# Performance work log

Measured on AMD Instinct MI355X. Metric: run time of the kernel, lower is better.

## Reference

```python
import jax, jax.numpy as jnp
import numpy as np

N_ATOMS = 50000
N_EDGES = 640000
RBF_DIM = 64
HIDDEN = 128


def setup_inputs() -> dict:
    key = jax.random.key(0)
    ks = jax.random.split(key, 12)
    s = 0.05
    return {
        "atom_feat": jax.random.normal(ks[0], (N_ATOMS, HIDDEN), jnp.float32),
        "pair_feat": jax.random.normal(ks[1], (N_EDGES, RBF_DIM), jnp.float32),
        "recv_idx": jax.random.randint(ks[2], (N_EDGES,), 0, N_ATOMS, jnp.int32),
        # dense_rbf: rbf_dim -> hidden
        "w_rbf": jax.random.normal(ks[3], (RBF_DIM, HIDDEN), jnp.float32) * s,
        "b_rbf": jnp.zeros((HIDDEN,), jnp.float32),
        # dense_pair: hidden -> hidden
        "w_pair": jax.random.normal(ks[4], (HIDDEN, HIDDEN), jnp.float32) * s,
        "b_pair": jnp.zeros((HIDDEN,), jnp.float32),
        # atom MLP: hidden -> hidden (swish) -> hidden
        "w1": jax.random.normal(ks[5], (HIDDEN, HIDDEN), jnp.float32) * s,
        "b1": jnp.zeros((HIDDEN,), jnp.float32),
        "w2": jax.random.normal(ks[6], (HIDDEN, HIDDEN), jnp.float32) * s,
        "b2": jnp.zeros((HIDDEN,), jnp.float32),
    }


def reference(atom_feat, pair_feat, recv_idx, w_rbf, b_rbf, w_pair, b_pair, w1, b1, w2, b2):
    # edge MLP: two linear layers (no activation, matching keras Dense defaults)
    edge_messages = pair_feat @ w_rbf + b_rbf            # [E, H]
    edge_messages = edge_messages @ w_pair + b_pair      # [E, H]
    # scatter-add edge messages onto receiving atoms
    aggregated = jax.ops.segment_sum(edge_messages, recv_idx, num_segments=atom_feat.shape[0])  # [N, H]
    # atom MLP with swish hidden activation + residual
    h = jax.nn.silu(aggregated @ w1 + b1)
    return atom_feat + (h @ w2 + b2)
```

## Files before the change

kernel.cpp:

```cpp
#include <hip/hip_runtime.h>
#include <hip/hip_bf16.h>

#define HID 128
#define RBF 64
#define CAP 40
#define APB 16

typedef __attribute__((ext_vector_type(8))) __bf16 bf16x8;
typedef __attribute__((ext_vector_type(4))) float  f32x4;

__device__ __forceinline__ int pack_off(int k, int j) {
    return (((k >> 5) * HID + j) * 4 + ((k >> 3) & 3)) * 8 + (k & 7);
}

__global__ __launch_bounds__(256) void k_prep(
    const float* __restrict__ w_rbf, const float* __restrict__ b_rbf,
    const float* __restrict__ w_pair, const float* __restrict__ b_pair,
    const float* __restrict__ w1, const float* __restrict__ w2,
    __bf16* __restrict__ wcp, float* __restrict__ b_comb,
    __bf16* __restrict__ w1p, __bf16* __restrict__ w2p,
    int* __restrict__ counts, int N)
{
    const int n4 = (N + 3) >> 2;
    const int e_zero = n4;
    const int e_wc   = e_zero + RBF * HID;
    const int e_bc   = e_wc + HID;
    const int e_w1   = e_bc + HID * HID;
    const int e_w2   = e_w1 + HID * HID;

    for (int i = blockIdx.x * 256 + threadIdx.x; i < e_w2; i += gridDim.x * 256) {
        if (i < e_zero) {
            int base = i * 4;
            if (base + 3 < N) reinterpret_cast<int4*>(counts)[i] = make_int4(0, 0, 0, 0);
            else for (int t = base; t < N; ++t) counts[t] = 0;
        } else if (i < e_wc) {
            int tid = i - e_zero;
            int k = tid >> 7, j = tid & (HID - 1);
            float acc = 0.f;
            #pragma unroll 8
            for (int l = 0; l < HID; ++l) acc += w_rbf[k * HID + l] * w_pair[l * HID + j];
            wcp[pack_off(k, j)] = (__bf16)acc;
        } else if (i < e_bc) {
            int j = i - e_wc;
            float acc = b_pair[j];
            #pragma unroll 8
            for (int l = 0; l < HID; ++l) acc += b_rbf[l] * w_pair[l * HID + j];
            b_comb[j] = acc;
        } else if (i < e_w1) {
            int tid = i - e_bc;
            int k = tid >> 7, j = tid & (HID - 1);
            w1p[pack_off(k, j)] = (__bf16)w1[tid];
        } else {
            int tid = i - e_w1;
            int k = tid >> 7, j = tid & (HID - 1);
            w2p[pack_off(k, j)] = (__bf16)w2[tid];
        }
    }
}

__global__ __launch_bounds__(256) void k_fill(
    const int* __restrict__ recv, int* counts, int* __restrict__ edge_list, int E)
{
    int e = blockIdx.x * 256 + threadIdx.x;
    if (e < E) {
        int r = recv[e];
        int slot = atomicAdd(&counts[r], 1);
        if (slot < CAP) edge_list[(size_t)r * CAP + slot] = e;
    }
}

__global__ __launch_bounds__(256) void k_fused(
    const float* __restrict__ pair_feat, const float* __restrict__ atom_feat,
    const int* __restrict__ counts, const int* __restrict__ edge_list,
    const __bf16* __restrict__ wcp, const float* __restrict__ bc,
    const __bf16* __restrict__ w1p, const float* __restrict__ b1,
    const __bf16* __restrict__ w2p, const float* __restrict__ b2,
    float* __restrict__ out, int n_atoms)
{
    __shared__ __bf16 s_lds[APB][RBF + 8];
    __shared__ __bf16 x_lds[APB][HID + 8];

    const int tid  = threadIdx.x;
    const int lane = tid & 63;
    const int wv   = tid >> 6;
    const int lo   = lane & 15;
    const int hi   = lane >> 4;
    const int a0   = blockIdx.x * APB;

    const int ab = a0 + wv * 4;
    int dq[4], eidq[4];
    #pragma unroll
    for (int q = 0; q < 4; ++q) {
        int a = ab + q;
        dq[q]   = (a < n_atoms) ? counts[a] : 0;
        eidq[q] = (lane < CAP && a < n_atoms) ? edge_list[(size_t)a * CAP + lane] : 0;
    }

    #pragma unroll
    for (int q = 0; q < 4; ++q) {
        int d = dq[q]; if (d > CAP) d = CAP;
        int eid = eidq[q];

        float acc0 = 0.f, acc1 = 0.f, acc2 = 0.f, acc3 = 0.f;
        float acc4 = 0.f, acc5 = 0.f, acc6 = 0.f, acc7 = 0.f;
        int p = 0;
        for (; p + 8 <= d; p += 8) {
            int e0 = __shfl(eid, p),     e1 = __shfl(eid, p + 1);
            int e2 = __shfl(eid, p + 2), e3 = __shfl(eid, p + 3);
            int e4 = __shfl(eid, p + 4), e5 = __shfl(eid, p + 5);
            int e6 = __shfl(eid, p + 6), e7 = __shfl(eid, p + 7);
            acc0 += pair_feat[(size_t)e0 * RBF + lane];
            acc1 += pair_feat[(size_t)e1 * RBF + lane];
            acc2 += pair_feat[(size_t)e2 * RBF + lane];
            acc3 += pair_feat[(size_t)e3 * RBF + lane];
            acc4 += pair_feat[(size_t)e4 * RBF + lane];
            acc5 += pair_feat[(size_t)e5 * RBF + lane];
            acc6 += pair_feat[(size_t)e6 * RBF + lane];
            acc7 += pair_feat[(size_t)e7 * RBF + lane];
        }
        if (p + 4 <= d) {
            int e0 = __shfl(eid, p),     e1 = __shfl(eid, p + 1);
            int e2 = __shfl(eid, p + 2), e3 = __shfl(eid, p + 3);
            acc0 += pair_feat[(size_t)e0 * RBF + lane];
            acc1 += pair_feat[(size_t)e1 * RBF + lane];
            acc2 += pair_feat[(size_t)e2 * RBF + lane];
            acc3 += pair_feat[(size_t)e3 * RBF + lane];
            p += 4;
        }
        if (p + 2 <= d) {
            int e0 = __shfl(eid, p), e1 = __shfl(eid, p + 1);
            acc4 += pair_feat[(size_t)e0 * RBF + lane];
            acc5 += pair_feat[(size_t)e1 * RBF + lane];
            p += 2;
        }
        if (p < d) {
            int e0 = __shfl(eid, p);
            acc6 += pair_feat[(size_t)e0 * RBF + lane];
        }
        s_lds[wv * 4 + q][lane] =
            (__bf16)(((acc0 + acc1) + (acc2 + acc3)) + ((acc4 + acc5) + (acc6 + acc7)));
    }
    __syncthreads();

    float dg[4];
    #pragma unroll
    for (int j = 0; j < 4; ++j) {
        int a = a0 + hi * 4 + j;
        dg[j] = (a < n_atoms) ? (float)counts[a] : 0.f;
    }

    bf16x8 sa0 = *reinterpret_cast<const bf16x8*>(&s_lds[lo][hi * 8]);
    bf16x8 sa1 = *reinterpret_cast<const bf16x8*>(&s_lds[lo][32 + hi * 8]);

    f32x4 acc[2];

    #pragma unroll
    for (int c = 0; c < 2; ++c) {
        int col = (wv * 2 + c) * 16 + lo;
        float bcv = bc[col];
        acc[c] = (f32x4){dg[0] * bcv, dg[1] * bcv, dg[2] * bcv, dg[3] * bcv};
        bf16x8 wb0 = *reinterpret_cast<const bf16x8*>(wcp + ((size_t)(0 * HID + col) * 4 + hi) * 8);
        bf16x8 wb1 = *reinterpret_cast<const bf16x8*>(wcp + ((size_t)(1 * HID + col) * 4 + hi) * 8);
        acc[c] = __builtin_amdgcn_mfma_f32_16x16x32_bf16(sa0, wb0, acc[c], 0, 0, 0);
        acc[c] = __builtin_amdgcn_mfma_f32_16x16x32_bf16(sa1, wb1, acc[c], 0, 0, 0);
    }
    #pragma unroll
    for (int c = 0; c < 2; ++c)
        #pragma unroll
        for (int j = 0; j < 4; ++j)
            x_lds[hi * 4 + j][(wv * 2 + c) * 16 + lo] = (__bf16)acc[c][j];
    __syncthreads();

    #pragma unroll
    for (int c = 0; c < 2; ++c) {
        float bv = b1[(wv * 2 + c) * 16 + lo];
        acc[c] = (f32x4){bv, bv, bv, bv};
    }
    #pragma unroll
    for (int t = 0; t < 4; ++t) {
        bf16x8 af = *reinterpret_cast<const bf16x8*>(&x_lds[lo][t * 32 + hi * 8]);
        #pragma unroll
        for (int c = 0; c < 2; ++c) {
            int col = (wv * 2 + c) * 16 + lo;
            bf16x8 bf = *reinterpret_cast<const bf16x8*>(
                w1p + ((size_t)(t * HID + col) * 4 + hi) * 8);
            acc[c] = __builtin_amdgcn_mfma_f32_16x16x32_bf16(af, bf, acc[c], 0, 0, 0);
        }
    }
    __syncthreads();

    #pragma unroll
    for (int c = 0; c < 2; ++c)
        #pragma unroll
        for (int j = 0; j < 4; ++j) {
            float z = acc[c][j];
            float h = z * (1.f / (1.f + __expf(-z)));
            x_lds[hi * 4 + j][(wv * 2 + c) * 16 + lo] = (__bf16)h;
        }
    __syncthreads();

    #pragma unroll
    for (int c = 0; c < 2; ++c) {
        float bv = b2[(wv * 2 + c) * 16 + lo];
        acc[c] = (f32x4){bv, bv, bv, bv};
    }
    #pragma unroll
    for (int t = 0; t < 4; ++t) {
        bf16x8 af = *reinterpret_cast<const bf16x8*>(&x_lds[lo][t * 32 + hi * 8]);
        #pragma unroll
        for (int c = 0; c < 2; ++c) {
            int col = (wv * 2 + c) * 16 + lo;
            bf16x8 bf = *reinterpret_cast<const bf16x8*>(
                w2p + ((size_t)(t * HID + col) * 4 + hi) * 8);
            acc[c] = __builtin_amdgcn_mfma_f32_16x16x32_bf16(af, bf, acc[c], 0, 0, 0);
        }
    }

    #pragma unroll
    for (int c = 0; c < 2; ++c)
        #pragma unroll
        for (int j = 0; j < 4; ++j) {
            int a = a0 + hi * 4 + j;
            if (a < n_atoms) {
                size_t idx = (size_t)a * HID + (wv * 2 + c) * 16 + lo;
                out[idx] = atom_feat[idx] + acc[c][j];
            }
        }
}

extern "C" void kernel_launch(void* const* d_in, const int* in_sizes, int n_in,
                              void* d_out, int out_size, void* d_ws, size_t ws_size,
                              hipStream_t stream)
{
    const float* atom_feat = (const float*)d_in[0];
    const float* pair_feat = (const float*)d_in[1];
    const int*   recv_idx  = (const int*)d_in[2];
    const float* w_rbf  = (const float*)d_in[3];
    const float* b_rbf  = (const float*)d_in[4];
    const float* w_pair = (const float*)d_in[5];
    const float* b_pair = (const float*)d_in[6];
    const float* w1     = (const float*)d_in[7];
    const float* b1     = (const float*)d_in[8];
    const float* w2     = (const float*)d_in[9];
    const float* b2     = (const float*)d_in[10];
    float* out = (float*)d_out;

    const int N = in_sizes[0] / HID;
    const int E = in_sizes[2];

    __bf16* wcp    = (__bf16*)d_ws;
    float*  b_comb = (float*)(wcp + RBF * HID);
    __bf16* w1p    = (__bf16*)(b_comb + HID);
    __bf16* w2p    = w1p + HID * HID;
    int* counts    = (int*)(w2p + HID * HID);
    int* edge_list = counts + N;

    const int prep_items = ((N + 3) >> 2) + RBF * HID + HID + 2 * HID * HID;

    k_prep<<<(prep_items + 255) / 256, 256, 0, stream>>>(
        w_rbf, b_rbf, w_pair, b_pair, w1, w2, wcp, b_comb, w1p, w2p, counts, N);
    k_fill<<<(E + 255) / 256, 256, 0, stream>>>(recv_idx, counts, edge_list, E);
    k_fused<<<(N + APB - 1) / APB, 256, 0, stream>>>(
        pair_feat, atom_feat, counts, edge_list,
        wcp, b_comb, w1p, b1, w2p, b2, out, N);
}
```

Measured before the change: 104.3 us.

## Scatter pair features as bf16 into per-atom slots instead of edge-index lists

The fill kernel now copies each edge's pair_feat row, converted to bf16, straight into a per-atom slot buffer while it claims slots with atomics. The fused kernel then reads those contiguous bf16 rows instead of doing random fp32 gathers through an edge list. The goal is to turn random gathers into streaming reads and to halve the bytes read in the fused kernel. In exchange the fill kernel reads all of pair_feat and writes a large N*CAP*RBF buffer, and the sums lose precision before accumulation.

```diff
diff --git a/kernel.cpp b/kernel.cpp
--- a/kernel.cpp
+++ b/kernel.cpp
@@ -5,8 +5,10 @@
 #define RBF 64
 #define CAP 40
 #define APB 16
+#define EPW 80
 
 typedef __attribute__((ext_vector_type(8))) __bf16 bf16x8;
+typedef __attribute__((ext_vector_type(4))) __bf16 bf16x4;
 typedef __attribute__((ext_vector_type(4))) float  f32x4;
 
 __device__ __forceinline__ int pack_off(int k, int j) {
@@ -58,20 +60,46 @@
     }
 }
 
-__global__ __launch_bounds__(256) void k_fill(
-    const int* __restrict__ recv, int* counts, int* __restrict__ edge_list, int E)
-{
-    int e = blockIdx.x * 256 + threadIdx.x;
-    if (e < E) {
-        int r = recv[e];
-        int slot = atomicAdd(&counts[r], 1);
-        if (slot < CAP) edge_list[(size_t)r * CAP + slot] = e;
+__global__ __launch_bounds__(256) void k_fillscatter(
+    const int* __restrict__ recv, const float* __restrict__ pair_feat,
+    int* counts, __bf16* __restrict__ gath, int E)
+{
+    const int lane = threadIdx.x & 63;
+    const int wv   = threadIdx.x >> 6;
+    const int wid  = blockIdx.x * 4 + wv;
+    const int g    = lane >> 4;
+    const int li   = lane & 15;
+
+    const int start = wid * EPW;
+    const int end0  = start + EPW;
+    const int end   = (end0 < E) ? end0 : E;
+
+    for (int e4 = start; e4 < end; e4 += 4) {
+        int r = 0, slot = CAP;
+        if (lane < 4) {
+            int e = e4 + lane;
+            if (e < end) {
+                r = recv[e];
+                slot = atomicAdd(&counts[r], 1);
+            }
+        }
+        int rg = __shfl(r, g);
+        int sg = __shfl(slot, g);
+        if (sg < CAP) {
+            f32x4 v = *reinterpret_cast<const f32x4*>(
+                pair_feat + (size_t)(e4 + g) * RBF + li * 4);
+            bf16x4 b;
+            #pragma unroll
+            for (int t = 0; t < 4; ++t) b[t] = (__bf16)v[t];
+            *reinterpret_cast<bf16x4*>(
+                gath + ((size_t)rg * CAP + sg) * RBF + li * 4) = b;
+        }
     }
 }
 
 __global__ __launch_bounds__(256) void k_fused(
-    const float* __restrict__ pair_feat, const float* __restrict__ atom_feat,
-    const int* __restrict__ counts, const int* __restrict__ edge_list,
+    const __bf16* __restrict__ gath, const float* __restrict__ atom_feat,
+    const int* __restrict__ counts,
     const __bf16* __restrict__ wcp, const float* __restrict__ bc,
     const __bf16* __restrict__ w1p, const float* __restrict__ b1,
     const __bf16* __restrict__ w2p, const float* __restrict__ b2,
@@ -88,54 +116,40 @@
     const int a0   = blockIdx.x * APB;
 
     const int ab = a0 + wv * 4;
-    int dq[4], eidq[4];
     #pragma unroll
     for (int q = 0; q < 4; ++q) {
         int a = ab + q;
-        dq[q]   = (a < n_atoms) ? counts[a] : 0;
-        eidq[q] = (lane < CAP && a < n_atoms) ? edge_list[(size_t)a * CAP + lane] : 0;
-    }
-
-    #pragma unroll
-    for (int q = 0; q < 4; ++q) {
-        int d = dq[q]; if (d > CAP) d = CAP;
-        int eid = eidq[q];
+        int d = 0;
+        if (a < n_atoms) { d = counts[a]; if (d > CAP) d = CAP; }
+        const __bf16* base = gath + (size_t)a * CAP * RBF;
 
         float acc0 = 0.f, acc1 = 0.f, acc2 = 0.f, acc3 = 0.f;
         float acc4 = 0.f, acc5 = 0.f, acc6 = 0.f, acc7 = 0.f;
         int p = 0;
         for (; p + 8 <= d; p += 8) {
-            int e0 = __shfl(eid, p),     e1 = __shfl(eid, p + 1);
-            int e2 = __shfl(eid, p + 2), e3 = __shfl(eid, p + 3);
-            int e4 = __shfl(eid, p + 4), e5 = __shfl(eid, p + 5);
-            int e6 = __shfl(eid, p + 6), e7 = __shfl(eid, p + 7);
-            acc0 += pair_feat[(size_t)e0 * RBF + lane];
-            acc1 += pair_feat[(size_t)e1 * RBF + lane];
-            acc2 += pair_feat[(size_t)e2 * RBF + lane];
-            acc3 += pair_feat[(size_t)e3 * RBF + lane];
-            acc4 += pair_feat[(size_t)e4 * RBF + lane];
-            acc5 += pair_feat[(size_t)e5 * RBF + lane];
-            acc6 += pair_feat[(size_t)e6 * RBF + lane];
-            acc7 += pair_feat[(size_t)e7 * RBF + lane];
+            acc0 += (float)base[(p + 0) * RBF + lane];
+            acc1 += (float)base[(p + 1) * RBF + lane];
+            acc2 += (float)base[(p + 2) * RBF + lane];
+            acc3 += (float)base[(p + 3) * RBF + lane];
+            acc4 += (float)base[(p + 4) * RBF + lane];
+            acc5 += (float)base[(p + 5) * RBF + lane];
+            acc6 += (float)base[(p + 6) * RBF + lane];
+            acc7 += (float)base[(p + 7) * RBF + lane];
         }
         if (p + 4 <= d) {
-            int e0 = __shfl(eid, p),     e1 = __shfl(eid, p + 1);
-            int e2 = __shfl(eid, p + 2), e3 = __shfl(eid, p + 3);
-            acc0 += pair_feat[(size_t)e0 * RBF + lane];
-            acc1 += pair_feat[(size_t)e1 * RBF + lane];
-            acc2 += pair_feat[(size_t)e2 * RBF + lane];
-            acc3 += pair_feat[(size_t)e3 * RBF + lane];
+            acc0 += (float)base[(p + 0) * RBF + lane];
+            acc1 += (float)base[(p + 1) * RBF + lane];
+            acc2 += (float)base[(p + 2) * RBF + lane];
+            acc3 += (float)base[(p + 3) * RBF + lane];
             p += 4;
         }
         if (p + 2 <= d) {
-            int e0 = __shfl(eid, p), e1 = __shfl(eid, p + 1);
-            acc4 += pair_feat[(size_t)e0 * RBF + lane];
-            acc5 += pair_feat[(size_t)e1 * RBF + lane];
+            acc4 += (float)base[(p + 0) * RBF + lane];
+            acc5 += (float)base[(p + 1) * RBF + lane];
             p += 2;
         }
         if (p < d) {
-            int e0 = __shfl(eid, p);
-            acc6 += pair_feat[(size_t)e0 * RBF + lane];
+            acc6 += (float)base[p * RBF + lane];
         }
         s_lds[wv * 4 + q][lane] =
             (__bf16)(((acc0 + acc1) + (acc2 + acc3)) + ((acc4 + acc5) + (acc6 + acc7)));
@@ -248,19 +262,22 @@
     const int N = in_sizes[0] / HID;
     const int E = in_sizes[2];
 
-    __bf16* wcp    = (__bf16*)d_ws;
-    float*  b_comb = (float*)(wcp + RBF * HID);
-    __bf16* w1p    = (__bf16*)(b_comb + HID);
-    __bf16* w2p    = w1p + HID * HID;
-    int* counts    = (int*)(w2p + HID * HID);
-    int* edge_list = counts + N;
+    char* w = (char*)d_ws;
+    __bf16* wcp    = (__bf16*)w;
+    float*  b_comb = (float*)(w + 16384);
+    __bf16* w1p    = (__bf16*)(w + 16896);
+    __bf16* w2p    = (__bf16*)(w + 49664);
+    int*    counts = (int*)(w + 82432);
+    size_t  goff   = (82432 + (size_t)N * 4 + 127) & ~(size_t)127;
+    __bf16* gath   = (__bf16*)(w + goff);
 
     const int prep_items = ((N + 3) >> 2) + RBF * HID + HID + 2 * HID * HID;
+    const int nwaves = (E + EPW - 1) / EPW;
+    const int nblk_fs = (nwaves + 3) / 4;
 
     k_prep<<<(prep_items + 255) / 256, 256, 0, stream>>>(
         w_rbf, b_rbf, w_pair, b_pair, w1, w2, wcp, b_comb, w1p, w2p, counts, N);
-    k_fill<<<(E + 255) / 256, 256, 0, stream>>>(recv_idx, counts, edge_list, E);
+    k_fillscatter<<<nblk_fs, 256, 0, stream>>>(recv_idx, pair_feat, counts, gath, E);
     k_fused<<<(N + APB - 1) / APB, 256, 0, stream>>>(
-        pair_feat, atom_feat, counts, edge_list,
-        wcp, b_comb, w1p, b1, w2p, b2, out, N);
-}
+        gath, atom_feat, counts, wcp, b_comb, w1p, b1, w2p, b2, out, N);
+}
```

New measurement: 118.3 us. +13.4%, slower.
